# Kernel tuning notes

Measured on AMD Instinct MI355X. Metric: run time of the kernel, lower is better.

Reference implementation:

```python
import jax, jax.numpy as jnp
import numpy as np
import math

NV, NC, NE = 25000, 12500, 250000
DV_LP = DC_LP = 16
D_IN = 128   # in_var_dim = in_con_dim = in_edge_dim
D_OUT = 128  # out_var_dim = out_con_dim = out_edge_dim
E_WO = 5
EDGE_IN = D_IN + 3 + E_WO       # 136 = num_edge_lp_f_with_ss(8) + in_edge_dim(128)
VAR_COMB = DV_LP + D_IN          # 144
CON_COMB = DC_LP + D_IN          # 144

def _lin(key, din, dout, bias=True):
    k1, k2 = jax.random.split(key)
    W = jax.random.normal(k1, (din, dout), jnp.float32) * 0.05
    if bias:
        return W, jax.random.normal(k2, (dout,), jnp.float32) * 0.05
    return W, None

def setup_inputs():
    key = jax.random.key(0)
    ks = iter(jax.random.split(key, 64))
    d = {}
    d["var_learned_f"] = jax.random.normal(next(ks), (NV, D_IN), jnp.float32)
    d["var_lp_f"] = jax.random.normal(next(ks), (NV, DV_LP), jnp.float32)
    d["con_learned_f"] = jax.random.normal(next(ks), (NC, D_IN), jnp.float32)
    d["con_lp_f"] = jax.random.normal(next(ks), (NC, DC_LP), jnp.float32)
    d["edge_learned_f"] = jax.random.normal(next(ks), (NE, D_IN), jnp.float32)
    d["lo_costs"] = jax.random.normal(next(ks), (NE,), jnp.float32)
    d["hi_costs"] = jax.random.normal(next(ks), (NE,), jnp.float32)
    d["def_mm"] = jax.random.normal(next(ks), (NE,), jnp.float32)
    d["edge_lp_f_wo_ss"] = jax.random.normal(next(ks), (NE, E_WO), jnp.float32)
    # con_updater TransformerConv: src=var_comb(144), dst=con_comb(144), edge(136) -> 128
    d["cu_Wq"], d["cu_bq"] = _lin(next(ks), CON_COMB, D_OUT)
    d["cu_Wk"], d["cu_bk"] = _lin(next(ks), VAR_COMB, D_OUT)
    d["cu_Wv"], d["cu_bv"] = _lin(next(ks), VAR_COMB, D_OUT)
    d["cu_We"], _ = _lin(next(ks), EDGE_IN, D_OUT, bias=False)
    d["cu_Ws"], d["cu_bs"] = _lin(next(ks), CON_COMB, D_OUT)
    # var_updater TransformerConv: src=new con_comb(144), dst=var_comb(144)
    d["vu_Wq"], d["vu_bq"] = _lin(next(ks), VAR_COMB, D_OUT)
    d["vu_Wk"], d["vu_bk"] = _lin(next(ks), CON_COMB, D_OUT)
    d["vu_Wv"], d["vu_bv"] = _lin(next(ks), CON_COMB, D_OUT)
    d["vu_We"], _ = _lin(next(ks), EDGE_IN, D_OUT, bias=False)
    d["vu_Ws"], d["vu_bs"] = _lin(next(ks), VAR_COMB, D_OUT)
    # EdgeUpdater MLPs (hidden = out_edge_dim = 128, num_hidden_layers_edge = 0)
    d["eu_vW1"], d["eu_vb1"] = _lin(next(ks), VAR_COMB, D_OUT)
    d["eu_vW2"], d["eu_vb2"] = _lin(next(ks), D_OUT, D_OUT)
    d["eu_cW1"], d["eu_cb1"] = _lin(next(ks), CON_COMB, D_OUT)
    d["eu_cW2"], d["eu_cb2"] = _lin(next(ks), D_OUT, D_OUT)
    d["eu_eW1"], d["eu_eb1"] = _lin(next(ks), EDGE_IN + 2 * D_OUT, D_OUT)
    d["eu_eW2"], d["eu_eb2"] = _lin(next(ks), D_OUT, D_OUT)
    d["edge_index_var"] = jax.random.randint(next(ks), (NE,), 0, NV)
    d["edge_index_con"] = jax.random.randint(next(ks), (NE,), 0, NC)
    return d

def transformer_conv(x_src, x_dst, src_idx, dst_idx, e,
                     Wq, bq, Wk, bk, Wv, bv, We, Ws, bs, n_dst):
    # PyG TransformerConv, heads=1, edge_dim, aggr='mean', root_weight=True
    C = Wq.shape[1]
    q = x_dst @ Wq + bq                      # [N_dst, C]
    k = x_src @ Wk + bk                      # [N_src, C]
    v = x_src @ Wv + bv
    ee = e @ We                              # [E, C] (lin_edge, no bias)
    kj = k[src_idx] + ee
    alpha = jnp.sum(q[dst_idx] * kj, axis=-1) * (1.0 / math.sqrt(C))  # [E]
    # segment softmax over destination nodes
    amax = jax.ops.segment_max(alpha, dst_idx, num_segments=n_dst)
    ex = jnp.exp(alpha - amax[dst_idx])
    denom = jax.ops.segment_sum(ex, dst_idx, num_segments=n_dst)
    a = ex / denom[dst_idx]
    msg = (v[src_idx] + ee) * a[:, None]
    agg = jax.ops.segment_sum(msg, dst_idx, num_segments=n_dst)
    cnt = jax.ops.segment_sum(jnp.ones_like(alpha), dst_idx, num_segments=n_dst)
    out = agg / jnp.maximum(cnt, 1.0)[:, None]   # aggr='mean'
    return out + x_dst @ Ws + bs                 # skip connection (lin_skip)

def _forward(var_learned_f, var_lp_f, con_learned_f, con_lp_f, edge_learned_f,
             lo_costs, hi_costs, def_mm, edge_lp_f_wo_ss,
             cu_Wq, cu_bq, cu_Wk, cu_bk, cu_Wv, cu_bv, cu_We, cu_Ws, cu_bs,
             vu_Wq, vu_bq, vu_Wk, vu_bk, vu_Wv, vu_bv, vu_We, vu_Ws, vu_bs,
             eu_vW1, eu_vb1, eu_vW2, eu_vb2, eu_cW1, eu_cb1, eu_cW2, eu_cb2,
             eu_eW1, eu_eb1, eu_eW2, eu_eb2,
             edge_index_var, edge_index_con):
    relu = jax.nn.relu
    var_comb = jnp.concatenate([var_learned_f, var_lp_f], axis=1)     # [NV,144]
    con_comb = jnp.concatenate([con_learned_f, con_lp_f], axis=1)     # [NC,144]
    edge_comb = jnp.concatenate([edge_learned_f, lo_costs[:, None], hi_costs[:, None],
                                 def_mm[:, None], edge_lp_f_wo_ss], axis=1)  # [NE,136]
    # con update: messages from vars (edge_index[0]) to cons (edge_index[1])
    con_new = relu(transformer_conv(var_comb, con_comb, edge_index_var, edge_index_con,
                                    edge_comb, cu_Wq, cu_bq, cu_Wk, cu_bk, cu_Wv, cu_bv,
                                    cu_We, cu_Ws, cu_bs, NC))
    con_comb = jnp.concatenate([con_new, con_lp_f], axis=1)
    # var update: flow target_to_source -> messages from cons (edge_index[1]) to vars (edge_index[0])
    var_new = relu(transformer_conv(con_comb, var_comb, edge_index_con, edge_index_var,
                                    edge_comb, vu_Wq, vu_bq, vu_Wk, vu_bk, vu_Wv, vu_bv,
                                    vu_We, vu_Ws, vu_bs, NV))
    var_comb = jnp.concatenate([var_new, var_lp_f], axis=1)
    # edge update: compress nodes, gather to edges, concat, MLP
    vc = relu(relu(var_comb @ eu_vW1 + eu_vb1) @ eu_vW2 + eu_vb2)     # [NV,128]
    cc = relu(relu(con_comb @ eu_cW1 + eu_cb1) @ eu_cW2 + eu_cb2)     # [NC,128]
    h = jnp.concatenate([edge_comb, vc[edge_index_var], cc[edge_index_con]], axis=1)  # [NE,392]
    edge_new = relu(relu(h @ eu_eW1 + eu_eb1) @ eu_eW2 + eu_eb2)
    return var_new, con_new, edge_new

def reference(var_learned_f, var_lp_f, con_learned_f, con_lp_f, edge_learned_f,
              lo_costs, hi_costs, def_mm, edge_lp_f_wo_ss,
              cu_Wq, cu_bq, cu_Wk, cu_bk, cu_Wv, cu_bv, cu_We, cu_Ws, cu_bs,
              vu_Wq, vu_bq, vu_Wk, vu_bk, vu_Wv, vu_bv, vu_We, vu_Ws, vu_bs,
              eu_vW1, eu_vb1, eu_vW2, eu_vb2, eu_cW1, eu_cb1, eu_cW2, eu_cb2,
              eu_eW1, eu_eb1, eu_eW2, eu_eb2,
              edge_index_var, edge_index_con):
    return _forward(var_learned_f, var_lp_f, con_learned_f, con_lp_f, edge_learned_f,
                    lo_costs, hi_costs, def_mm, edge_lp_f_wo_ss,
                    cu_Wq, cu_bq, cu_Wk, cu_bk, cu_Wv, cu_bv, cu_We, cu_Ws, cu_bs,
                    vu_Wq, vu_bq, vu_Wk, vu_bk, vu_Wv, vu_bv, vu_We, vu_Ws, vu_bs,
                    eu_vW1, eu_vb1, eu_vW2, eu_vb2, eu_cW1, eu_cb1, eu_cW2, eu_cb2,
                    eu_eW1, eu_eb1, eu_eW2, eu_eb2,
                    edge_index_var, edge_index_con)
```

## Files before the change

kernel.cpp:

```cpp
#include <hip/hip_runtime.h>
#include <math.h>

#define NVV 25000
#define NCC 12500
#define NEE 250000
#define KP 160

typedef short bf16x8 __attribute__((ext_vector_type(8)));
typedef float f32x4 __attribute__((ext_vector_type(4)));

__device__ __forceinline__ unsigned short f2bf(float f) {
  unsigned u = __float_as_uint(f);
  u += 0x7fffu + ((u >> 16) & 1u);
  return (unsigned short)(u >> 16);
}
__device__ __forceinline__ float bf2f(unsigned short u) {
  return __uint_as_float((unsigned)u << 16);
}
__device__ __forceinline__ void gll16(const unsigned short* g, unsigned short* l) {
  __builtin_amdgcn_global_load_lds(
      (const __attribute__((address_space(1))) unsigned int*)(const void*)g,
      (__attribute__((address_space(3))) unsigned int*)(void*)l, 16, 0, 0);
}

__device__ __forceinline__ void stage_rows64(const unsigned short* __restrict__ X,
                                             unsigned short* As, int row0, int N,
                                             int wave, int lane) {
  #pragma unroll
  for (int j = 0; j < 5; ++j) {
    int inst = wave * 5 + j;
    int L = inst * 1024 + lane * 16;
    int kk = L >> 12;
    int r = (L >> 6) & 63;
    int ks = (L & 63) >> 1;
    int grow = row0 + r; if (grow >= N) grow = N - 1;
    gll16(X + (size_t)grow * KP + kk * 32 + ks, As + inst * 512);
  }
}

template <int MI, int NI>
__device__ __forceinline__ void zero_acc(f32x4 (&acc)[MI][NI]) {
  #pragma unroll
  for (int mi = 0; mi < MI; ++mi)
    #pragma unroll
    for (int ni = 0; ni < NI; ++ni) {
      acc[mi][ni][0] = 0.f; acc[mi][ni][1] = 0.f;
      acc[mi][ni][2] = 0.f; acc[mi][ni][3] = 0.f;
    }
}

template <int MI, int NI>
__device__ __forceinline__ void chunk_mfma_g(const unsigned short* As,
                                             const unsigned short* __restrict__ WT,
                                             f32x4 (&acc)[MI][NI], int kk,
                                             int wm, int wn, int fr, int fq) {
  bf16x8 av[MI], bv[NI];
  #pragma unroll
  for (int mi = 0; mi < MI; ++mi)
    av[mi] = *(const bf16x8*)&As[kk * 2048 + (wm + mi * 16 + fr) * 32 + fq * 8];
  #pragma unroll
  for (int ni = 0; ni < NI; ++ni)
    bv[ni] = *(const bf16x8*)&WT[(size_t)(wn + ni * 16 + fr) * KP + kk * 32 + fq * 8];
  #pragma unroll
  for (int mi = 0; mi < MI; ++mi)
    #pragma unroll
    for (int ni = 0; ni < NI; ++ni)
      acc[mi][ni] = __builtin_amdgcn_mfma_f32_16x16x32_bf16(av[mi], bv[ni],
                                                            acc[mi][ni], 0, 0, 0);
}

struct GJob {
  const unsigned short* X; const unsigned short* WT;
  const float* bias; const float* addf;
  float* outf; unsigned short* outb;
  int outb_stride, pad_flag, N, relu_flag;
};
struct GBatch { GJob j[4]; int start[4]; int njobs; };

__global__ __launch_bounds__(256, 5) void gemm_batch(GBatch B) {
  int job = 0;
  #pragma unroll
  for (int t = 1; t < 4; ++t)
    if (t < B.njobs && (int)blockIdx.x >= B.start[t]) job = t;
  GJob g = B.j[job];
  __shared__ unsigned short As[5 * 64 * 32];
  const int tid = threadIdx.x;
  const int lane = tid & 63, wave = tid >> 6;
  const int row0 = (blockIdx.x - B.start[job]) * 64;
  const int wm = (wave & 1) * 32, wn = (wave >> 1) * 64;
  const int fr = lane & 15, fq = lane >> 4;

  stage_rows64(g.X, As, row0, g.N, wave, lane);
  f32x4 acc[2][4];
  zero_acc<2, 4>(acc);
  __syncthreads();
  #pragma unroll
  for (int kk = 0; kk < 5; ++kk) chunk_mfma_g<2, 4>(As, g.WT, acc, kk, wm, wn, fr, fq);

  #pragma unroll
  for (int mi = 0; mi < 2; ++mi) {
    #pragma unroll
    for (int ni = 0; ni < 4; ++ni) {
      int gcol = wn + ni * 16 + fr;
      float bvv = g.bias ? g.bias[gcol] : 0.0f;
      #pragma unroll
      for (int r = 0; r < 4; ++r) {
        int grow = row0 + wm + mi * 16 + fq * 4 + r;
        if (grow < g.N) {
          float o = acc[mi][ni][r] + bvv;
          if (g.addf) o += g.addf[(size_t)grow * 128 + gcol];
          if (g.relu_flag) o = fmaxf(o, 0.f);
          if (g.outf) g.outf[(size_t)grow * 128 + gcol] = o;
          if (g.outb) g.outb[(size_t)grow * g.outb_stride + gcol] = f2bf(o);
        }
      }
    }
    if (g.outb && g.pad_flag && wn == 0) {
      #pragma unroll
      for (int r = 0; r < 4; ++r) {
        int grow = row0 + wm + mi * 16 + fq * 4 + r;
        if (grow < g.N)
          for (int pc = 128 + fr; pc < g.outb_stride; pc += 16)
            g.outb[(size_t)grow * g.outb_stride + pc] = 0;
      }
    }
  }
}

__global__ __launch_bounds__(256, 4) void gemm_t(
    const unsigned short* __restrict__ X, const unsigned short* __restrict__ WT,
    unsigned short* __restrict__ outb, int N) {
  __shared__ unsigned short As[5 * 64 * 32];
  const int tid = threadIdx.x;
  const int lane = tid & 63, wave = tid >> 6;
  const int row0 = blockIdx.x * 64;
  const int wm = (wave & 1) * 32, wn = (wave >> 1) * 80;
  const int fr = lane & 15, fq = lane >> 4;

  stage_rows64(X, As, row0, N, wave, lane);
  f32x4 acc[2][5];
  zero_acc<2, 5>(acc);
  __syncthreads();
  #pragma unroll
  for (int kk = 0; kk < 5; ++kk) chunk_mfma_g<2, 5>(As, WT, acc, kk, wm, wn, fr, fq);

  #pragma unroll
  for (int mi = 0; mi < 2; ++mi)
    #pragma unroll
    for (int ni = 0; ni < 5; ++ni) {
      int gcol = wn + ni * 16 + fr;
      #pragma unroll
      for (int r = 0; r < 4; ++r) {
        int grow = row0 + wm + mi * 16 + fq * 4 + r;
        if (grow < N) outb[(size_t)grow * KP + gcol] = f2bf(acc[mi][ni][r]);
      }
    }
}

__global__ __launch_bounds__(256, 5) void gemm_chain(
    const unsigned short* __restrict__ X,
    const unsigned short* __restrict__ W1, const float* __restrict__ b1,
    const unsigned short* __restrict__ gA, const unsigned short* __restrict__ gB,
    const int* __restrict__ giA, const int* __restrict__ giB,
    const unsigned short* __restrict__ W2, const float* __restrict__ b2,
    const unsigned short* __restrict__ W3, const float* __restrict__ b3,
    float* __restrict__ outf, unsigned short* __restrict__ outw,
    int N, int relu_last) {
  __shared__ unsigned short As[5 * 64 * 32];
  const int tid = threadIdx.x;
  const int lane = tid & 63, wave = tid >> 6;
  const int row0 = blockIdx.x * 64;
  const int wm = (wave & 1) * 32, wn = (wave >> 1) * 64;
  const int fr = lane & 15, fq = lane >> 4;

  stage_rows64(X, As, row0, N, wave, lane);
  f32x4 acc[2][4];
  zero_acc<2, 4>(acc);
  __syncthreads();
  #pragma unroll
  for (int kk = 0; kk < 5; ++kk) chunk_mfma_g<2, 4>(As, W1, acc, kk, wm, wn, fr, fq);

  __syncthreads();
  #pragma unroll
  for (int mi = 0; mi < 2; ++mi) {
    #pragma unroll
    for (int ni = 0; ni < 4; ++ni) {
      int col = wn + ni * 16 + fr;
      float bvv = b1 ? b1[col] : 0.0f;
      #pragma unroll
      for (int r = 0; r < 4; ++r) {
        int row = wm + mi * 16 + fq * 4 + r;
        int grow = row0 + row;
        int gi = (grow < N) ? grow : (N - 1);
        float o = acc[mi][ni][r] + bvv;
        if (gA) o += bf2f(gA[(size_t)giA[gi] * 128 + col]) +
                     bf2f(gB[(size_t)giB[gi] * 128 + col]);
        o = fmaxf(o, 0.f);
        As[(col >> 5) * 2048 + row * 32 + (col & 31)] = f2bf(o);
      }
    }
  }
  zero_acc<2, 4>(acc);
  __syncthreads();

  #pragma unroll
  for (int kk = 0; kk < 4; ++kk) chunk_mfma_g<2, 4>(As, W2, acc, kk, wm, wn, fr, fq);

  if (W3) {
    __syncthreads();
    #pragma unroll
    for (int mi = 0; mi < 2; ++mi) {
      #pragma unroll
      for (int ni = 0; ni < 4; ++ni) {
        int col = wn + ni * 16 + fr;
        float bvv = b2 ? b2[col] : 0.0f;
        #pragma unroll
        for (int r = 0; r < 4; ++r) {
          int row = wm + mi * 16 + fq * 4 + r;
          float o = fmaxf(acc[mi][ni][r] + bvv, 0.f);
          As[(col >> 5) * 2048 + row * 32 + (col & 31)] = f2bf(o);
        }
      }
    }
    zero_acc<2, 4>(acc);
    __syncthreads();
    #pragma unroll
    for (int kk = 0; kk < 4; ++kk) chunk_mfma_g<2, 4>(As, W3, acc, kk, wm, wn, fr, fq);
    #pragma unroll
    for (int mi = 0; mi < 2; ++mi)
      #pragma unroll
      for (int ni = 0; ni < 4; ++ni) {
        int gcol = wn + ni * 16 + fr;
        float bvv = b3 ? b3[gcol] : 0.0f;
        #pragma unroll
        for (int r = 0; r < 4; ++r) {
          int grow = row0 + wm + mi * 16 + fq * 4 + r;
          if (grow < N) {
            float o = acc[mi][ni][r] + bvv;
            if (relu_last) o = fmaxf(o, 0.f);
            if (outw) outw[(size_t)grow * 128 + gcol] = f2bf(o);
            else      __builtin_nontemporal_store(o, &outf[(size_t)grow * 128 + gcol]);
          }
        }
      }
  } else {
    #pragma unroll
    for (int mi = 0; mi < 2; ++mi)
      #pragma unroll
      for (int ni = 0; ni < 4; ++ni) {
        int gcol = wn + ni * 16 + fr;
        float bvv = b2 ? b2[gcol] : 0.0f;
        #pragma unroll
        for (int r = 0; r < 4; ++r) {
          int grow = row0 + wm + mi * 16 + fq * 4 + r;
          if (grow < N) {
            float o = acc[mi][ni][r] + bvv;
            if (relu_last) o = fmaxf(o, 0.f);
            if (outw) outw[(size_t)grow * 128 + gcol] = f2bf(o);
            else      __builtin_nontemporal_store(o, &outf[(size_t)grow * 128 + gcol]);
          }
        }
      }
  }
}

__global__ void build_node_bf(const float* __restrict__ learned, const float* __restrict__ lp,
                              unsigned short* __restrict__ out, int N) {
  int idx = blockIdx.x * blockDim.x + threadIdx.x;
  if (idx >= N * 40) return;
  int row = idx / 40, c4 = idx - row * 40;
  int c = c4 * 4;
  ushort4 o;
  if (c4 < 32) {
    const float* p = learned + (size_t)row * 128 + c;
    o.x = f2bf(p[0]); o.y = f2bf(p[1]); o.z = f2bf(p[2]); o.w = f2bf(p[3]);
  } else if (c4 < 36) {
    const float* p = lp + (size_t)row * 16 + (c - 128);
    o.x = f2bf(p[0]); o.y = f2bf(p[1]); o.z = f2bf(p[2]); o.w = f2bf(p[3]);
  } else { o.x = o.y = o.z = o.w = 0; }
  *(ushort4*)&out[(size_t)row * KP + c] = o;
}

__global__ void build_edge_bf(const float* __restrict__ el, const float* __restrict__ lo,
                              const float* __restrict__ hi, const float* __restrict__ dm,
                              const float* __restrict__ wo, unsigned short* __restrict__ out) {
  int idx = blockIdx.x * blockDim.x + threadIdx.x;
  if (idx >= NEE * 40) return;
  int row = idx / 40, c4 = idx - row * 40;
  int c = c4 * 4;
  ushort4 o;
  if (c4 < 32) {
    const float* p = el + (size_t)row * 128 + c;
    o.x = f2bf(p[0]); o.y = f2bf(p[1]); o.z = f2bf(p[2]); o.w = f2bf(p[3]);
  } else if (c4 == 32) {
    o.x = f2bf(lo[row]); o.y = f2bf(hi[row]); o.z = f2bf(dm[row]);
    o.w = f2bf(wo[(size_t)row * 5 + 0]);
  } else if (c4 == 33) {
    const float* p = wo + (size_t)row * 5;
    o.x = f2bf(p[1]); o.y = f2bf(p[2]); o.z = f2bf(p[3]); o.w = f2bf(p[4]);
  } else { o.x = o.y = o.z = o.w = 0; }
  *(ushort4*)&out[(size_t)row * KP + c] = o;
}

struct WJobs {
  const float* W[20];
  unsigned short* O[20];
  int K[20];
  int TR[20];
};
__global__ void convert_weights(WJobs j) {
  int b = blockIdx.x;
  int job = b / 100;
  int i = (b - job * 100) * 256 + threadIdx.x;
  int col = i / KP;
  int k = i - col * KP;
  float v = 0.f;
  if (j.TR[job]) { if (col < 128 && k < j.K[job]) v = j.W[job][(size_t)k * 128 + col]; }
  else           { if (col < 136 && k < j.K[job]) v = j.W[job][(size_t)col * 128 + k]; }
  j.O[job][(size_t)col * KP + k] = f2bf(v);
}

__global__ void zero2(int* __restrict__ a, int na, int* __restrict__ b, int nb) {
  int i = blockIdx.x * blockDim.x + threadIdx.x;
  if (i < na) a[i] = 0;
  if (i < nb) b[i] = 0;
}
__global__ void hist2(const int* __restrict__ dc, int* __restrict__ cc,
                      const int* __restrict__ dv, int* __restrict__ cv, int nE) {
  int e = blockIdx.x * blockDim.x + threadIdx.x;
  if (e >= nE) return;
  atomicAdd(&cc[dc[e]], 1);
  atomicAdd(&cv[dv[e]], 1);
}
__global__ void csr_scan(const int* __restrict__ counts, int* __restrict__ offsets,
                         int* __restrict__ cursor, int n) {
  __shared__ int part[256];
  int tid = threadIdx.x;
  int chunk = (n + 255) / 256;
  int lo = tid * chunk, hi = min(n, lo + chunk);
  int s = 0;
  for (int i = lo; i < hi; ++i) s += counts[i];
  part[tid] = s;
  __syncthreads();
  if (tid == 0) {
    int run = 0;
    for (int i = 0; i < 256; ++i) { int t = part[i]; part[i] = run; run += t; }
    offsets[n] = run;
  }
  __syncthreads();
  int base = part[tid];
  for (int i = lo; i < hi; ++i) { offsets[i] = base; cursor[i] = base; base += counts[i]; }
}
__global__ void csr_scatter(const int* __restrict__ dst, const int* __restrict__ src,
                            int* __restrict__ cursor, int2* __restrict__ ces, int nE) {
  int e = blockIdx.x * blockDim.x + threadIdx.x;
  if (e >= nE) return;
  int pos = atomicAdd(&cursor[dst[e]], 1);
  ces[pos] = make_int2(e, src[e]);
}

struct AttSt { float m, l, ax, ay, axe, aye, axe2, aye2; };
__device__ __forceinline__ void att_upd(AttSt& s, float alpha, unsigned vu,
                                        float e0, float e1, float e2, float e3) {
  float mn = fmaxf(s.m, alpha);
  float scale = __expf(s.m - mn);
  float w = __expf(alpha - mn);
  s.ax = s.ax * scale + __uint_as_float(vu << 16) * w;
  s.ay = s.ay * scale + __uint_as_float(vu & 0xffff0000u) * w;
  s.axe = s.axe * scale + e0 * w;   s.aye = s.aye * scale + e1 * w;
  s.axe2 = s.axe2 * scale + e2 * w; s.aye2 = s.aye2 * scale + e3 * w;
  s.l = s.l * scale + w; s.m = mn;
}

__global__ void fused_attn(
    const float* __restrict__ qbuf, const unsigned short* __restrict__ kbuf,
    const unsigned short* __restrict__ vbuf, const unsigned short* __restrict__ tbuf,
    const unsigned short* __restrict__ ecomb,
    const int* __restrict__ offsets, const int2* __restrict__ ces,
    float* __restrict__ accVS, unsigned short* __restrict__ accE, int Nd) {
  int d = blockIdx.x * 4 + (threadIdx.x >> 6);
  if (d >= Nd) return;
  int lane = threadIdx.x & 63;
  int c = lane * 2;
  bool tl = (lane < 16);
  int c2 = 128 + c;
  float2 qv = *(const float2*)&qbuf[(size_t)d * 128 + c];
  unsigned tu = *(const unsigned*)&tbuf[(size_t)d * KP + c];
  float tx = __uint_as_float(tu << 16);
  float ty = __uint_as_float(tu & 0xffff0000u);
  float tx2 = 0.f, ty2 = 0.f;
  if (tl) {
    unsigned tu2 = *(const unsigned*)&tbuf[(size_t)d * KP + c2];
    tx2 = __uint_as_float(tu2 << 16);
    ty2 = __uint_as_float(tu2 & 0xffff0000u);
  }
  int beg = offsets[d], end = offsets[d + 1];
  AttSt st{-INFINITY, 0.f, 0.f, 0.f, 0.f, 0.f, 0.f, 0.f};
  const float SC = 0.08838834764831845f;
  int i = beg;
  for (; i + 3 < end; i += 4) {
    int2 pr[4];
    pr[0] = ces[i]; pr[1] = ces[i + 1]; pr[2] = ces[i + 2]; pr[3] = ces[i + 3];
    unsigned eu[4], ku[4], vu[4];
    float e0[4], e1[4], e2[4], e3[4], p[4];
    #pragma unroll
    for (int u = 0; u < 4; ++u) {
      eu[u] = *(const unsigned*)&ecomb[(size_t)pr[u].x * KP + c];
      ku[u] = *(const unsigned*)&kbuf[(size_t)pr[u].y * 128 + c];
      vu[u] = *(const unsigned*)&vbuf[(size_t)pr[u].y * 128 + c];
    }
    #pragma unroll
    for (int u = 0; u < 4; ++u) {
      e0[u] = __uint_as_float(eu[u] << 16);
      e1[u] = __uint_as_float(eu[u] & 0xffff0000u);
      e2[u] = 0.f; e3[u] = 0.f;
    }
    if (tl) {
      #pragma unroll
      for (int u = 0; u < 4; ++u) {
        unsigned x = *(const unsigned*)&ecomb[(size_t)pr[u].x * KP + c2];
        e2[u] = __uint_as_float(x << 16);
        e3[u] = __uint_as_float(x & 0xffff0000u);
      }
    }
    #pragma unroll
    for (int u = 0; u < 4; ++u)
      p[u] = qv.x * __uint_as_float(ku[u] << 16) + qv.y * __uint_as_float(ku[u] & 0xffff0000u)
           + tx * e0[u] + ty * e1[u] + tx2 * e2[u] + ty2 * e3[u];
    #pragma unroll
    for (int off = 1; off < 64; off <<= 1) {
      p[0] += __shfl_xor(p[0], off, 64);
      p[1] += __shfl_xor(p[1], off, 64);
      p[2] += __shfl_xor(p[2], off, 64);
      p[3] += __shfl_xor(p[3], off, 64);
    }
    #pragma unroll
    for (int u = 0; u < 4; ++u)
      att_upd(st, p[u] * SC, vu[u], e0[u], e1[u], e2[u], e3[u]);
  }
  for (; i < end; ++i) {
    int2 pr = ces[i];
    unsigned eu = *(const unsigned*)&ecomb[(size_t)pr.x * KP + c];
    float e0 = __uint_as_float(eu << 16);
    float e1 = __uint_as_float(eu & 0xffff0000u);
    float e2 = 0.f, e3 = 0.f;
    if (tl) {
      unsigned x = *(const unsigned*)&ecomb[(size_t)pr.x * KP + c2];
      e2 = __uint_as_float(x << 16);
      e3 = __uint_as_float(x & 0xffff0000u);
    }
    unsigned ku = *(const unsigned*)&kbuf[(size_t)pr.y * 128 + c];
    unsigned vu = *(const unsigned*)&vbuf[(size_t)pr.y * 128 + c];
    float p = qv.x * __uint_as_float(ku << 16) + qv.y * __uint_as_float(ku & 0xffff0000u)
            + tx * e0 + ty * e1 + tx2 * e2 + ty2 * e3;
    #pragma unroll
    for (int off = 1; off < 64; off <<= 1) p += __shfl_xor(p, off, 64);
    att_upd(st, p * SC, vu, e0, e1, e2, e3);
  }
  int deg = end - beg;
  float inv = (deg > 0) ? 1.0f / (st.l * (float)deg) : 0.0f;
  float2 sk = *(const float2*)&accVS[(size_t)d * 128 + c];
  *(float2*)&accVS[(size_t)d * 128 + c] =
      make_float2(st.ax * inv + sk.x, st.ay * inv + sk.y);
  ushort2 oe; oe.x = f2bf(st.axe * inv); oe.y = f2bf(st.aye * inv);
  *(ushort2*)&accE[(size_t)d * KP + c] = oe;
  if (tl) {
    ushort2 oe2; oe2.x = f2bf(st.axe2 * inv); oe2.y = f2bf(st.aye2 * inv);
    *(ushort2*)&accE[(size_t)d * KP + c2] = oe2;
  }
}

extern "C" void kernel_launch(void* const* d_in, const int* in_sizes, int n_in,
                              void* d_out, int out_size, void* d_ws, size_t ws_size,
                              hipStream_t stream) {
  const float* var_learned = (const float*)d_in[0];
  const float* var_lp      = (const float*)d_in[1];
  const float* con_learned = (const float*)d_in[2];
  const float* con_lp      = (const float*)d_in[3];
  const float* edge_learned= (const float*)d_in[4];
  const float* lo          = (const float*)d_in[5];
  const float* hi          = (const float*)d_in[6];
  const float* dm          = (const float*)d_in[7];
  const float* wo          = (const float*)d_in[8];
  const float* cu_Wq = (const float*)d_in[9],  *cu_bq = (const float*)d_in[10];
  const float* cu_Wk = (const float*)d_in[11], *cu_bk = (const float*)d_in[12];
  const float* cu_Wv = (const float*)d_in[13], *cu_bv = (const float*)d_in[14];
  const float* cu_We = (const float*)d_in[15];
  const float* cu_Ws = (const float*)d_in[16], *cu_bs = (const float*)d_in[17];
  const float* vu_Wq = (const float*)d_in[18], *vu_bq = (const float*)d_in[19];
  const float* vu_Wk = (const float*)d_in[20], *vu_bk = (const float*)d_in[21];
  const float* vu_Wv = (const float*)d_in[22], *vu_bv = (const float*)d_in[23];
  const float* vu_We = (const float*)d_in[24];
  const float* vu_Ws = (const float*)d_in[25], *vu_bs = (const float*)d_in[26];
  const float* eu_vW1 = (const float*)d_in[27], *eu_vb1 = (const float*)d_in[28];
  const float* eu_vW2 = (const float*)d_in[29], *eu_vb2 = (const float*)d_in[30];
  const float* eu_cW1 = (const float*)d_in[31], *eu_cb1 = (const float*)d_in[32];
  const float* eu_cW2 = (const float*)d_in[33], *eu_cb2 = (const float*)d_in[34];
  const float* eu_eW1 = (const float*)d_in[35], *eu_eb1 = (const float*)d_in[36];
  const float* eu_eW2 = (const float*)d_in[37], *eu_eb2 = (const float*)d_in[38];
  const int* eiv = (const int*)d_in[39];
  const int* eic = (const int*)d_in[40];

  float* out_var  = (float*)d_out;
  float* out_con  = out_var + (size_t)NVV * 128;
  float* out_edge = out_con + (size_t)NCC * 128;

  char* w = (char*)d_ws;
  auto alloc = [&](size_t bytes) { char* p = w; w += (bytes + 255) & ~(size_t)255; return p; };
  unsigned short* edge_comb_bf = (unsigned short*)alloc((size_t)NEE * KP * 2);
  unsigned short* var_comb_bf = (unsigned short*)alloc((size_t)NVV * KP * 2);
  unsigned short* con_comb_bf = (unsigned short*)alloc((size_t)NCC * KP * 2);
  unsigned short* q_bf    = (unsigned short*)alloc((size_t)NVV * KP * 2);
  unsigned short* t_bf    = (unsigned short*)alloc((size_t)NVV * KP * 2);
  unsigned short* accE_bf = (unsigned short*)alloc((size_t)NVV * KP * 2);
  unsigned short* kv_bf   = (unsigned short*)alloc((size_t)NVV * 128 * 2);
  unsigned short* vv_bf   = (unsigned short*)alloc((size_t)NVV * 128 * 2);
  unsigned short* vc_bf   = (unsigned short*)alloc((size_t)NVV * 128 * 2);
  unsigned short* cc_bf   = (unsigned short*)alloc((size_t)NCC * 128 * 2);
  float* bufV1 = (float*)alloc((size_t)NVV * 128 * 4);
  float* bufV2 = (float*)alloc((size_t)NVV * 128 * 4);
  float* bufC1 = (float*)alloc((size_t)NCC * 128 * 4);
  float* bufC2 = (float*)alloc((size_t)NCC * 128 * 4);
  unsigned short* WTbase = (unsigned short*)alloc((size_t)20 * 160 * KP * 2);
  int* countsC = (int*)alloc((size_t)NCC * 4);
  int* countsV = (int*)alloc((size_t)NVV * 4);
  int* offC = (int*)alloc((size_t)(NCC + 1) * 4);
  int* curC = (int*)alloc((size_t)NCC * 4);
  int* offV = (int*)alloc((size_t)(NVV + 1) * 4);
  int* curV = (int*)alloc((size_t)NVV * 4);
  int2* cesA = (int2*)alloc((size_t)NEE * 8);
  int2* cesB = (int2*)alloc((size_t)NEE * 8);
  (void)ws_size; (void)in_sizes; (void)n_in; (void)out_size;

  unsigned short* WT[20];
  for (int i = 0; i < 20; ++i) WT[i] = WTbase + (size_t)i * 160 * KP;
  WJobs jobs;
  const float* Wsrc[20] = {cu_Wq, cu_Wk, cu_Wv, cu_We, cu_Ws,
                           vu_Wq, vu_Wk, vu_Wv, vu_We, vu_Ws,
                           eu_vW1, eu_vW2, eu_cW1, eu_cW2,
                           eu_eW1, eu_eW1 + 136 * 128, eu_eW1 + 264 * 128, eu_eW2,
                           cu_We, vu_We};
  const int Ksrc[20] = {144, 144, 144, 136, 144, 144, 144, 144, 136, 144,
                        144, 128, 144, 128, 136, 128, 128, 128, 128, 128};
  const int Tsrc[20] = {1,1,1,1,1, 1,1,1,1,1, 1,1,1,1, 1,1,1,1, 0,0};
  for (int i = 0; i < 20; ++i) {
    jobs.W[i] = Wsrc[i]; jobs.O[i] = WT[i]; jobs.K[i] = Ksrc[i]; jobs.TR[i] = Tsrc[i];
  }

  const int T = 256;
  const int NBC = (NCC + 63) / 64;
  const int NBV = (NVV + 63) / 64;
  const int NBE = (NEE + 63) / 64;

  build_node_bf<<<(NVV * 40 + T - 1) / T, T, 0, stream>>>(var_learned, var_lp, var_comb_bf, NVV);
  build_node_bf<<<(NCC * 40 + T - 1) / T, T, 0, stream>>>(con_learned, con_lp, con_comb_bf, NCC);
  build_edge_bf<<<(NEE * 40 + T - 1) / T, T, 0, stream>>>(edge_learned, lo, hi, dm, wo, edge_comb_bf);
  convert_weights<<<20 * 100, T, 0, stream>>>(jobs);

  zero2<<<(NVV + T - 1) / T, T, 0, stream>>>(countsC, NCC, countsV, NVV);
  hist2<<<(NEE + T - 1) / T, T, 0, stream>>>(eic, countsC, eiv, countsV, NEE);
  csr_scan<<<1, 256, 0, stream>>>(countsC, offC, curC, NCC);
  csr_scan<<<1, 256, 0, stream>>>(countsV, offV, curV, NVV);
  csr_scatter<<<(NEE + T - 1) / T, T, 0, stream>>>(eic, eiv, curC, cesA, NEE);
  csr_scatter<<<(NEE + T - 1) / T, T, 0, stream>>>(eiv, eic, curV, cesB, NEE);

  {
    GBatch b{};
    b.j[0] = {con_comb_bf, WT[0], cu_bq, nullptr, bufC1, q_bf, KP, 1, NCC, 0};
    b.j[1] = {con_comb_bf, WT[4], cu_bs, nullptr, bufC2, nullptr, 0, 0, NCC, 0};
    b.j[2] = {var_comb_bf, WT[1], cu_bk, nullptr, nullptr, kv_bf, 128, 0, NVV, 0};
    b.j[3] = {var_comb_bf, WT[2], cu_bv, nullptr, nullptr, vv_bf, 128, 0, NVV, 0};
    b.start[0] = 0; b.start[1] = NBC; b.start[2] = 2 * NBC; b.start[3] = 2 * NBC + NBV;
    b.njobs = 4;
    gemm_batch<<<2 * NBC + 2 * NBV, 256, 0, stream>>>(b);
  }
  gemm_t<<<NBC, 256, 0, stream>>>(q_bf, WT[18], t_bf, NCC);
  fused_attn<<<(NCC + 3) / 4, 256, 0, stream>>>(bufC1, kv_bf, vv_bf, t_bf, edge_comb_bf,
                                                offC, cesA, bufC2, accE_bf, NCC);
  {
    GBatch b{};
    b.j[0] = {accE_bf, WT[3], nullptr, bufC2, out_con, con_comb_bf, KP, 0, NCC, 1};
    b.start[0] = 0; b.njobs = 1;
    gemm_batch<<<NBC, 256, 0, stream>>>(b);
  }

  {
    GBatch b{};
    b.j[0] = {var_comb_bf, WT[5], vu_bq, nullptr, bufV1, q_bf, KP, 1, NVV, 0};
    b.j[1] = {var_comb_bf, WT[9], vu_bs, nullptr, bufV2, nullptr, 0, 0, NVV, 0};
    b.j[2] = {con_comb_bf, WT[6], vu_bk, nullptr, nullptr, kv_bf, 128, 0, NCC, 0};
    b.j[3] = {con_comb_bf, WT[7], vu_bv, nullptr, nullptr, vv_bf, 128, 0, NCC, 0};
    b.start[0] = 0; b.start[1] = NBV; b.start[2] = 2 * NBV; b.start[3] = 2 * NBV + NBC;
    b.njobs = 4;
    gemm_batch<<<2 * NBV + 2 * NBC, 256, 0, stream>>>(b);
  }
  gemm_t<<<NBV, 256, 0, stream>>>(q_bf, WT[19], t_bf, NVV);
  fused_attn<<<(NVV + 3) / 4, 256, 0, stream>>>(bufV1, kv_bf, vv_bf, t_bf, edge_comb_bf,
                                                offV, cesB, bufV2, accE_bf, NVV);
  {
    GBatch b{};
    b.j[0] = {accE_bf, WT[8], nullptr, bufV2, out_var, var_comb_bf, KP, 0, NVV, 1};
    b.start[0] = 0; b.njobs = 1;
    gemm_batch<<<NBV, 256, 0, stream>>>(b);
  }

  gemm_chain<<<NBV, 256, 0, stream>>>(
      var_comb_bf, WT[10], eu_vb1, nullptr, nullptr, nullptr, nullptr,
      WT[11], eu_vb2, WT[15], nullptr, nullptr, vc_bf, NVV, 0);
  gemm_chain<<<NBC, 256, 0, stream>>>(
      con_comb_bf, WT[12], eu_cb1, nullptr, nullptr, nullptr, nullptr,
      WT[13], eu_cb2, WT[16], nullptr, nullptr, cc_bf, NCC, 0);
  gemm_chain<<<NBE, 256, 0, stream>>>(
      edge_comb_bf, WT[14], eu_eb1, vc_bf, cc_bf, eiv, eic,
      WT[17], eu_eb2, nullptr, nullptr, out_edge, nullptr, NEE, 1);
}
```

Measured before the change: 831.7 us.

## Fuse Q and T projections for both updaters, prefetch second tile in edge MLP

```diff
diff --git a/kernel.cpp b/kernel.cpp
--- a/kernel.cpp
+++ b/kernel.cpp
@@ -74,10 +74,11 @@
   const float* bias; const float* addf;
   float* outf; unsigned short* outb;
   int outb_stride, pad_flag, N, relu_flag;
+  int ntf;
 };
 struct GBatch { GJob j[4]; int start[4]; int njobs; };
 
-__global__ __launch_bounds__(256, 5) void gemm_batch(GBatch B) {
+__global__ __launch_bounds__(256, 4) void gemm_batch(GBatch B) {
   int job = 0;
   #pragma unroll
   for (int t = 1; t < 4; ++t)
@@ -110,7 +111,10 @@
           float o = acc[mi][ni][r] + bvv;
           if (g.addf) o += g.addf[(size_t)grow * 128 + gcol];
           if (g.relu_flag) o = fmaxf(o, 0.f);
-          if (g.outf) g.outf[(size_t)grow * 128 + gcol] = o;
+          if (g.outf) {
+            if (g.ntf) __builtin_nontemporal_store(o, &g.outf[(size_t)grow * 128 + gcol]);
+            else       g.outf[(size_t)grow * 128 + gcol] = o;
+          }
           if (g.outb) g.outb[(size_t)grow * g.outb_stride + gcol] = f2bf(o);
         }
       }
@@ -127,45 +131,74 @@
   }
 }
 
-__global__ __launch_bounds__(256, 4) void gemm_t(
-    const unsigned short* __restrict__ X, const unsigned short* __restrict__ WT,
-    unsigned short* __restrict__ outb, int N) {
+struct QTJob {
+  const unsigned short* X; const unsigned short* Wq; const float* bq;
+  const unsigned short* Wt; float* qf; unsigned short* tb; int N;
+};
+struct QTBatch { QTJob j[2]; int start; };
+
+__global__ __launch_bounds__(256, 4) void gemm_qt(QTBatch B) {
+  int job = ((int)blockIdx.x >= B.start) ? 1 : 0;
+  QTJob g = B.j[job];
   __shared__ unsigned short As[5 * 64 * 32];
   const int tid = threadIdx.x;
   const int lane = tid & 63, wave = tid >> 6;
-  const int row0 = blockIdx.x * 64;
-  const int wm = (wave & 1) * 32, wn = (wave >> 1) * 80;
+  const int row0 = (blockIdx.x - (job ? B.start : 0)) * 64;
+  const int wm = (wave & 1) * 32;
   const int fr = lane & 15, fq = lane >> 4;
 
-  stage_rows64(X, As, row0, N, wave, lane);
-  f32x4 acc[2][5];
-  zero_acc<2, 5>(acc);
-  __syncthreads();
-  #pragma unroll
-  for (int kk = 0; kk < 5; ++kk) chunk_mfma_g<2, 5>(As, WT, acc, kk, wm, wn, fr, fq);
-
-  #pragma unroll
-  for (int mi = 0; mi < 2; ++mi)
-    #pragma unroll
-    for (int ni = 0; ni < 5; ++ni) {
-      int gcol = wn + ni * 16 + fr;
-      #pragma unroll
-      for (int r = 0; r < 4; ++r) {
-        int grow = row0 + wm + mi * 16 + fq * 4 + r;
-        if (grow < N) outb[(size_t)grow * KP + gcol] = f2bf(acc[mi][ni][r]);
-      }
-    }
-}
-
-__global__ __launch_bounds__(256, 5) void gemm_chain(
+  stage_rows64(g.X, As, row0, g.N, wave, lane);
+  {
+    const int wn = (wave >> 1) * 64;
+    f32x4 acc[2][4];
+    zero_acc<2, 4>(acc);
+    __syncthreads();
+    #pragma unroll
+    for (int kk = 0; kk < 5; ++kk) chunk_mfma_g<2, 4>(As, g.Wq, acc, kk, wm, wn, fr, fq);
+    __syncthreads();
+    #pragma unroll
+    for (int mi = 0; mi < 2; ++mi)
+      #pragma unroll
+      for (int ni = 0; ni < 4; ++ni) {
+        int col = wn + ni * 16 + fr;
+        float bvv = g.bq[col];
+        #pragma unroll
+        for (int r = 0; r < 4; ++r) {
+          int row = wm + mi * 16 + fq * 4 + r;
+          int grow = row0 + row;
+          float o = acc[mi][ni][r] + bvv;
+          if (grow < g.N) g.qf[(size_t)grow * 128 + col] = o;
+          As[(col >> 5) * 2048 + row * 32 + (col & 31)] = f2bf(o);
+        }
+      }
+  }
+  __syncthreads();
+  {
+    const int wn = (wave >> 1) * 80;
+    f32x4 acc[2][5];
+    zero_acc<2, 5>(acc);
+    #pragma unroll
+    for (int kk = 0; kk < 4; ++kk) chunk_mfma_g<2, 5>(As, g.Wt, acc, kk, wm, wn, fr, fq);
+    #pragma unroll
+    for (int mi = 0; mi < 2; ++mi)
+      #pragma unroll
+      for (int ni = 0; ni < 5; ++ni) {
+        int gcol = wn + ni * 16 + fr;
+        #pragma unroll
+        for (int r = 0; r < 4; ++r) {
+          int grow = row0 + wm + mi * 16 + fq * 4 + r;
+          if (grow < g.N) g.tb[(size_t)grow * KP + gcol] = f2bf(acc[mi][ni][r]);
+        }
+      }
+  }
+}
+
+__global__ __launch_bounds__(256, 4) void gemm_chain(
     const unsigned short* __restrict__ X,
     const unsigned short* __restrict__ W1, const float* __restrict__ b1,
-    const unsigned short* __restrict__ gA, const unsigned short* __restrict__ gB,
-    const int* __restrict__ giA, const int* __restrict__ giB,
     const unsigned short* __restrict__ W2, const float* __restrict__ b2,
-    const unsigned short* __restrict__ W3, const float* __restrict__ b3,
-    float* __restrict__ outf, unsigned short* __restrict__ outw,
-    int N, int relu_last) {
+    const unsigned short* __restrict__ W3,
+    unsigned short* __restrict__ outw, int N) {
   __shared__ unsigned short As[5 * 64 * 32];
   const int tid = threadIdx.x;
   const int lane = tid & 63, wave = tid >> 6;
@@ -182,86 +215,140 @@
 
   __syncthreads();
   #pragma unroll
-  for (int mi = 0; mi < 2; ++mi) {
+  for (int mi = 0; mi < 2; ++mi)
     #pragma unroll
     for (int ni = 0; ni < 4; ++ni) {
       int col = wn + ni * 16 + fr;
-      float bvv = b1 ? b1[col] : 0.0f;
+      float bvv = b1[col];
       #pragma unroll
       for (int r = 0; r < 4; ++r) {
         int row = wm + mi * 16 + fq * 4 + r;
-        int grow = row0 + row;
+        float o = fmaxf(acc[mi][ni][r] + bvv, 0.f);
+        As[(col >> 5) * 2048 + row * 32 + (col & 31)] = f2bf(o);
+      }
+    }
+  zero_acc<2, 4>(acc);
+  __syncthreads();
+
+  #pragma unroll
+  for (int kk = 0; kk < 4; ++kk) chunk_mfma_g<2, 4>(As, W2, acc, kk, wm, wn, fr, fq);
+
+  __syncthreads();
+  #pragma unroll
+  for (int mi = 0; mi < 2; ++mi)
+    #pragma unroll
+    for (int ni = 0; ni < 4; ++ni) {
+      int col = wn + ni * 16 + fr;
+      float bvv = b2[col];
+      #pragma unroll
+      for (int r = 0; r < 4; ++r) {
+        int row = wm + mi * 16 + fq * 4 + r;
+        float o = fmaxf(acc[mi][ni][r] + bvv, 0.f);
+        As[(col >> 5) * 2048 + row * 32 + (col & 31)] = f2bf(o);
+      }
+    }
+  zero_acc<2, 4>(acc);
+  __syncthreads();
+  #pragma unroll
+  for (int kk = 0; kk < 4; ++kk) chunk_mfma_g<2, 4>(As, W3, acc, kk, wm, wn, fr, fq);
+  #pragma unroll
+  for (int mi = 0; mi < 2; ++mi)
+    #pragma unroll
+    for (int ni = 0; ni < 4; ++ni) {
+      int gcol = wn + ni * 16 + fr;
+      #pragma unroll
+      for (int r = 0; r < 4; ++r) {
+        int grow = row0 + wm + mi * 16 + fq * 4 + r;
+        if (grow < N) outw[(size_t)grow * 128 + gcol] = f2bf(acc[mi][ni][r]);
+      }
+    }
+}
+
+__device__ __forceinline__ void edge_epi(unsigned short* L, const f32x4 (&acc)[2][4],
+    int rbase, int N, const float* __restrict__ b1,
+    const unsigned short* __restrict__ gA, const unsigned short* __restrict__ gB,
+    const int* __restrict__ giA, const int* __restrict__ giB,
+    int wm, int wn, int fr, int fq) {
+  #pragma unroll
+  for (int mi = 0; mi < 2; ++mi)
+    #pragma unroll
+    for (int ni = 0; ni < 4; ++ni) {
+      int col = wn + ni * 16 + fr;
+      float bvv = b1[col];
+      #pragma unroll
+      for (int r = 0; r < 4; ++r) {
+        int row = wm + mi * 16 + fq * 4 + r;
+        int grow = rbase + row;
         int gi = (grow < N) ? grow : (N - 1);
-        float o = acc[mi][ni][r] + bvv;
-        if (gA) o += bf2f(gA[(size_t)giA[gi] * 128 + col]) +
-                     bf2f(gB[(size_t)giB[gi] * 128 + col]);
+        float o = acc[mi][ni][r] + bvv
+                + bf2f(gA[(size_t)giA[gi] * 128 + col])
+                + bf2f(gB[(size_t)giB[gi] * 128 + col]);
         o = fmaxf(o, 0.f);
-        As[(col >> 5) * 2048 + row * 32 + (col & 31)] = f2bf(o);
-      }
-    }
-  }
+        L[(col >> 5) * 2048 + row * 32 + (col & 31)] = f2bf(o);
+      }
+    }
+}
+__device__ __forceinline__ void edge_store(const f32x4 (&acc)[2][4], int rbase, int N,
+    const float* __restrict__ b2, float* __restrict__ outf,
+    int wm, int wn, int fr, int fq) {
+  #pragma unroll
+  for (int mi = 0; mi < 2; ++mi)
+    #pragma unroll
+    for (int ni = 0; ni < 4; ++ni) {
+      int gcol = wn + ni * 16 + fr;
+      float bvv = b2[gcol];
+      #pragma unroll
+      for (int r = 0; r < 4; ++r) {
+        int grow = rbase + wm + mi * 16 + fq * 4 + r;
+        if (grow < N) {
+          float o = fmaxf(acc[mi][ni][r] + bvv, 0.f);
+          __builtin_nontemporal_store(o, &outf[(size_t)grow * 128 + gcol]);
+        }
+      }
+    }
+}
+
+__global__ __launch_bounds__(256, 4) void gemm_edge2(
+    const unsigned short* __restrict__ X,
+    const unsigned short* __restrict__ W1, const float* __restrict__ b1,
+    const unsigned short* __restrict__ gA, const unsigned short* __restrict__ gB,
+    const int* __restrict__ giA, const int* __restrict__ giB,
+    const unsigned short* __restrict__ W2, const float* __restrict__ b2,
+    float* __restrict__ outf, int N) {
+  __shared__ unsigned short As[5 * 64 * 32];
+  __shared__ unsigned short Bs[5 * 64 * 32];
+  const int tid = threadIdx.x;
+  const int lane = tid & 63, wave = tid >> 6;
+  const int row0 = blockIdx.x * 128;
+  const int wm = (wave & 1) * 32, wn = (wave >> 1) * 64;
+  const int fr = lane & 15, fq = lane >> 4;
+
+  stage_rows64(X, As, row0, N, wave, lane);
+  f32x4 acc[2][4];
   zero_acc<2, 4>(acc);
   __syncthreads();
-
+  stage_rows64(X, Bs, row0 + 64, N, wave, lane);
+
+  #pragma unroll
+  for (int kk = 0; kk < 5; ++kk) chunk_mfma_g<2, 4>(As, W1, acc, kk, wm, wn, fr, fq);
+  __syncthreads();
+  edge_epi(As, acc, row0, N, b1, gA, gB, giA, giB, wm, wn, fr, fq);
+  zero_acc<2, 4>(acc);
+  __syncthreads();
   #pragma unroll
   for (int kk = 0; kk < 4; ++kk) chunk_mfma_g<2, 4>(As, W2, acc, kk, wm, wn, fr, fq);
-
-  if (W3) {
-    __syncthreads();
-    #pragma unroll
-    for (int mi = 0; mi < 2; ++mi) {
-      #pragma unroll
-      for (int ni = 0; ni < 4; ++ni) {
-        int col = wn + ni * 16 + fr;
-        float bvv = b2 ? b2[col] : 0.0f;
-        #pragma unroll
-        for (int r = 0; r < 4; ++r) {
-          int row = wm + mi * 16 + fq * 4 + r;
-          float o = fmaxf(acc[mi][ni][r] + bvv, 0.f);
-          As[(col >> 5) * 2048 + row * 32 + (col & 31)] = f2bf(o);
-        }
-      }
-    }
-    zero_acc<2, 4>(acc);
-    __syncthreads();
-    #pragma unroll
-    for (int kk = 0; kk < 4; ++kk) chunk_mfma_g<2, 4>(As, W3, acc, kk, wm, wn, fr, fq);
-    #pragma unroll
-    for (int mi = 0; mi < 2; ++mi)
-      #pragma unroll
-      for (int ni = 0; ni < 4; ++ni) {
-        int gcol = wn + ni * 16 + fr;
-        float bvv = b3 ? b3[gcol] : 0.0f;
-        #pragma unroll
-        for (int r = 0; r < 4; ++r) {
-          int grow = row0 + wm + mi * 16 + fq * 4 + r;
-          if (grow < N) {
-            float o = acc[mi][ni][r] + bvv;
-            if (relu_last) o = fmaxf(o, 0.f);
-            if (outw) outw[(size_t)grow * 128 + gcol] = f2bf(o);
-            else      __builtin_nontemporal_store(o, &outf[(size_t)grow * 128 + gcol]);
-          }
-        }
-      }
-  } else {
-    #pragma unroll
-    for (int mi = 0; mi < 2; ++mi)
-      #pragma unroll
-      for (int ni = 0; ni < 4; ++ni) {
-        int gcol = wn + ni * 16 + fr;
-        float bvv = b2 ? b2[gcol] : 0.0f;
-        #pragma unroll
-        for (int r = 0; r < 4; ++r) {
-          int grow = row0 + wm + mi * 16 + fq * 4 + r;
-          if (grow < N) {
-            float o = acc[mi][ni][r] + bvv;
-            if (relu_last) o = fmaxf(o, 0.f);
-            if (outw) outw[(size_t)grow * 128 + gcol] = f2bf(o);
-            else      __builtin_nontemporal_store(o, &outf[(size_t)grow * 128 + gcol]);
-          }
-        }
-      }
-  }
+  edge_store(acc, row0, N, b2, outf, wm, wn, fr, fq);
+
+  zero_acc<2, 4>(acc);
+  #pragma unroll
+  for (int kk = 0; kk < 5; ++kk) chunk_mfma_g<2, 4>(Bs, W1, acc, kk, wm, wn, fr, fq);
+  __syncthreads();
+  edge_epi(Bs, acc, row0 + 64, N, b1, gA, gB, giA, giB, wm, wn, fr, fq);
+  zero_acc<2, 4>(acc);
+  __syncthreads();
+  #pragma unroll
+  for (int kk = 0; kk < 4; ++kk) chunk_mfma_g<2, 4>(Bs, W2, acc, kk, wm, wn, fr, fq);
+  edge_store(acc, row0 + 64, N, b2, outf, wm, wn, fr, fq);
 }
 
 __global__ void build_node_bf(const float* __restrict__ learned, const float* __restrict__ lp,
@@ -510,8 +597,8 @@
   unsigned short* edge_comb_bf = (unsigned short*)alloc((size_t)NEE * KP * 2);
   unsigned short* var_comb_bf = (unsigned short*)alloc((size_t)NVV * KP * 2);
   unsigned short* con_comb_bf = (unsigned short*)alloc((size_t)NCC * KP * 2);
-  unsigned short* q_bf    = (unsigned short*)alloc((size_t)NVV * KP * 2);
-  unsigned short* t_bf    = (unsigned short*)alloc((size_t)NVV * KP * 2);
+  unsigned short* t_bfA   = (unsigned short*)alloc((size_t)NCC * KP * 2);
+  unsigned short* t_bfB   = (unsigned short*)alloc((size_t)NVV * KP * 2);
   unsigned short* accE_bf = (unsigned short*)alloc((size_t)NVV * KP * 2);
   unsigned short* kv_bf   = (unsigned short*)alloc((size_t)NVV * 128 * 2);
   unsigned short* vv_bf   = (unsigned short*)alloc((size_t)NVV * 128 * 2);
@@ -550,7 +637,7 @@
   const int T = 256;
   const int NBC = (NCC + 63) / 64;
   const int NBV = (NVV + 63) / 64;
-  const int NBE = (NEE + 63) / 64;
+  const int NBE2 = (NEE + 127) / 128;
 
   build_node_bf<<<(NVV * 40 + T - 1) / T, T, 0, stream>>>(var_learned, var_lp, var_comb_bf, NVV);
   build_node_bf<<<(NCC * 40 + T - 1) / T, T, 0, stream>>>(con_learned, con_lp, con_comb_bf, NCC);
@@ -565,52 +652,54 @@
   csr_scatter<<<(NEE + T - 1) / T, T, 0, stream>>>(eiv, eic, curV, cesB, NEE);
 
   {
+    QTBatch b{};
+    b.j[0] = {con_comb_bf, WT[0], cu_bq, WT[18], bufC1, t_bfA, NCC};
+    b.j[1] = {var_comb_bf, WT[5], vu_bq, WT[19], bufV1, t_bfB, NVV};
+    b.start = NBC;
+    gemm_qt<<<NBC + NBV, 256, 0, stream>>>(b);
+  }
+
+  {
     GBatch b{};
-    b.j[0] = {con_comb_bf, WT[0], cu_bq, nullptr, bufC1, q_bf, KP, 1, NCC, 0};
-    b.j[1] = {con_comb_bf, WT[4], cu_bs, nullptr, bufC2, nullptr, 0, 0, NCC, 0};
-    b.j[2] = {var_comb_bf, WT[1], cu_bk, nullptr, nullptr, kv_bf, 128, 0, NVV, 0};
-    b.j[3] = {var_comb_bf, WT[2], cu_bv, nullptr, nullptr, vv_bf, 128, 0, NVV, 0};
-    b.start[0] = 0; b.start[1] = NBC; b.start[2] = 2 * NBC; b.start[3] = 2 * NBC + NBV;
-    b.njobs = 4;
-    gemm_batch<<<2 * NBC + 2 * NBV, 256, 0, stream>>>(b);
-  }
-  gemm_t<<<NBC, 256, 0, stream>>>(q_bf, WT[18], t_bf, NCC);
-  fused_attn<<<(NCC + 3) / 4, 256, 0, stream>>>(bufC1, kv_bf, vv_bf, t_bf, edge_comb_bf,
+    b.j[0] = {con_comb_bf, WT[4], cu_bs, nullptr, bufC2, nullptr, 0, 0, NCC, 0, 0};
+    b.j[1] = {var_comb_bf, WT[1], cu_bk, nullptr, nullptr, kv_bf, 128, 0, NVV, 0, 0};
+    b.j[2] = {var_comb_bf, WT[2], cu_bv, nullptr, nullptr, vv_bf, 128, 0, NVV, 0, 0};
+    b.start[0] = 0; b.start[1] = NBC; b.start[2] = NBC + NBV;
+    b.njobs = 3;
+    gemm_batch<<<NBC + 2 * NBV, 256, 0, stream>>>(b);
+  }
+  fused_attn<<<(NCC + 3) / 4, 256, 0, stream>>>(bufC1, kv_bf, vv_bf, t_bfA, edge_comb_bf,
                                                 offC, cesA, bufC2, accE_bf, NCC);
   {
     GBatch b{};
-    b.j[0] = {accE_bf, WT[3], nullptr, bufC2, out_con, con_comb_bf, KP, 0, NCC, 1};
+    b.j[0] = {accE_bf, WT[3], nullptr, bufC2, out_con, con_comb_bf, KP, 0, NCC, 1, 1};
     b.start[0] = 0; b.njobs = 1;
     gemm_batch<<<NBC, 256, 0, stream>>>(b);
   }
 
   {
     GBatch b{};
-    b.j[0] = {var_comb_bf, WT[5], vu_bq, nullptr, bufV1, q_bf, KP, 1, NVV, 0};
-    b.j[1] = {var_comb_bf, WT[9], vu_bs, nullptr, bufV2, nullptr, 0, 0, NVV, 0};
-    b.j[2] = {con_comb_bf, WT[6], vu_bk, nullptr, nullptr, kv_bf, 128, 0, NCC, 0};
-    b.j[3] = {con_comb_bf, WT[7], vu_bv, nullptr, nullptr, vv_bf, 128, 0, NCC, 0};
-    b.start[0] = 0; b.start[1] = NBV; b.start[2] = 2 * NBV; b.start[3] = 2 * NBV + NBC;
-    b.njobs = 4;
-    gemm_batch<<<2 * NBV + 2 * NBC, 256, 0, stream>>>(b);
-  }
-  gemm_t<<<NBV, 256, 0, stream>>>(q_bf, WT[19], t_bf, NVV);
-  fused_attn<<<(NVV + 3) / 4, 256, 0, stream>>>(bufV1, kv_bf, vv_bf, t_bf, edge_comb_bf,
+    b.j[0] = {var_comb_bf, WT[9], vu_bs, nullptr, bufV2, nullptr, 0, 0, NVV, 0, 0};
+    b.j[1] = {con_comb_bf, WT[6], vu_bk, nullptr, nullptr, kv_bf, 128, 0, NCC, 0, 0};
+    b.j[2] = {con_comb_bf, WT[7], vu_bv, nullptr, nullptr, vv_bf, 128, 0, NCC, 0, 0};
+    b.start[0] = 0; b.start[1] = NBV; b.start[2] = NBV + NBC;
+    b.njobs = 3;
+    gemm_batch<<<NBV + 2 * NBC, 256, 0, stream>>>(b);
+  }
+  fused_attn<<<(NVV + 3) / 4, 256, 0, stream>>>(bufV1, kv_bf, vv_bf, t_bfB, edge_comb_bf,
                                                 offV, cesB, bufV2, accE_bf, NVV);
   {
     GBatch b{};
-    b.j[0] = {accE_bf, WT[8], nullptr, bufV2, out_var, var_comb_bf, KP, 0, NVV, 1};
+    b.j[0] = {accE_bf, WT[8], nullptr, bufV2, out_var, var_comb_bf, KP, 0, NVV, 1, 1};
     b.start[0] = 0; b.njobs = 1;
     gemm_batch<<<NBV, 256, 0, stream>>>(b);
   }
 
   gemm_chain<<<NBV, 256, 0, stream>>>(
-      var_comb_bf, WT[10], eu_vb1, nullptr, nullptr, nullptr, nullptr,
-      WT[11], eu_vb2, WT[15], nullptr, nullptr, vc_bf, NVV, 0);
+      var_comb_bf, WT[10], eu_vb1, WT[11], eu_vb2, WT[15], vc_bf, NVV);
   gemm_chain<<<NBC, 256, 0, stream>>>(
-      con_comb_bf, WT[12], eu_cb1, nullptr, nullptr, nullptr, nullptr,
-      WT[13], eu_cb2, WT[16], nullptr, nullptr, cc_bf, NCC, 0);
-  gemm_chain<<<NBE, 256, 0, stream>>>(
+      con_comb_bf, WT[12], eu_cb1, WT[13], eu_cb2, WT[16], cc_bf, NCC);
+  gemm_edge2<<<NBE2, 256, 0, stream>>>(
       edge_comb_bf, WT[14], eu_eb1, vc_bf, cc_bf, eiv, eic,
-      WT[17], eu_eb2, nullptr, nullptr, out_edge, nullptr, NEE, 1);
-}
+      WT[17], eu_eb2, out_edge, NEE);
+}
```

New measurement: 775.3 us. 1.07x faster.
